# Kernel tuning notes

Hardware: AMD Instinct MI355X
Metric: run time of the kernel (lower is better)

## Reference

```python
import jax, jax.numpy as jnp
import numpy as np

N, R, E, EDIM = 500_000, 200, 1_000_000, 128


def setup_inputs() -> dict:
    key = jax.random.key(0)
    k = jax.random.split(key, 7)
    return {
        "emb": jax.random.normal(k[0], (N, EDIM), dtype=jnp.float32),
        "relations": jax.random.normal(k[1], (R, EDIM), dtype=jnp.float32),
        "tokeys": jax.random.normal(k[2], (EDIM, EDIM), dtype=jnp.float32) / np.sqrt(EDIM).astype(np.float32),
        "toqueries": jax.random.normal(k[3], (EDIM, EDIM), dtype=jnp.float32) / np.sqrt(EDIM).astype(np.float32),
        "si": jax.random.randint(k[4], (E,), 0, N),
        "pi": jax.random.randint(k[5], (E,), 0, R),
        "oi": jax.random.randint(k[6], (E,), 0, N),
    }


def reference(emb, relations, tokeys, toqueries, si, pi, oi):
    # emb: (N, e); relations: (R, e); tokeys/toqueries: (e, e); si/pi/oi: (E,)
    e = emb.shape[1]
    # einsum('ij, nj -> ni', W, x)  ==  x @ W.T
    semb = jnp.einsum('ij,nj->ni', tokeys, emb[si])      # (E, e)
    oemb = jnp.einsum('ij,nj->ni', toqueries, emb[oi])   # (E, e)
    pemb = relations[pi]                                  # (E, e)
    dots = jnp.sum(semb * pemb * oemb, axis=1) / jnp.sqrt(jnp.asarray(e, semb.dtype))
    return dots
```

## Files before the change

kernel.cpp:

```cpp
#include <hip/hip_runtime.h>
#include <hip/hip_bf16.h>

typedef __bf16 bf16x8 __attribute__((ext_vector_type(8)));
typedef float  f32x4  __attribute__((ext_vector_type(4)));

#define EDGES_TOTAL 1000000
#define TILE_E 16
#define TILES (EDGES_TOTAL / TILE_E)
#define EMB_ELEMS 64000000ULL
#define EMB_CHUNKS (EMB_ELEMS / 8)
#define WS_NEEDED (EMB_ELEMS * 2ULL)
#define GRID_BLOCKS 1280

__device__ __forceinline__ bf16x8 load_cvt8(const float* __restrict__ p) {
    f32x4 a = *(const f32x4*)p;
    f32x4 b = *(const f32x4*)(p + 4);
    bf16x8 r;
    r[0] = (__bf16)a[0]; r[1] = (__bf16)a[1]; r[2] = (__bf16)a[2]; r[3] = (__bf16)a[3];
    r[4] = (__bf16)b[0]; r[5] = (__bf16)b[1]; r[6] = (__bf16)b[2]; r[7] = (__bf16)b[3];
    return r;
}

__device__ __forceinline__ void gload_lds16(const void* g, void* l) {
    __builtin_amdgcn_global_load_lds(
        (const __attribute__((address_space(1))) void*)g,
        (__attribute__((address_space(3))) void*)l, 16, 0, 0);
}

__global__ __launch_bounds__(256) void cvt_bf16(
    const float* __restrict__ emb, __bf16* __restrict__ dst)
{
    const size_t stride = (size_t)gridDim.x * blockDim.x;
    for (size_t i = (size_t)blockIdx.x * blockDim.x + threadIdx.x; i < EMB_CHUNKS; i += stride) {
        size_t e = i * 8;
        *(bf16x8*)(dst + e) = load_cvt8(emb + e);
    }
}

__global__ __launch_bounds__(256, 5) void sampleall_staged(
    const __bf16* __restrict__ embb, const float* __restrict__ rel,
    const float* __restrict__ tokeys, const float* __restrict__ toqueries,
    const int* __restrict__ si, const int* __restrict__ pi, const int* __restrict__ oi,
    float* __restrict__ out)
{
    __shared__ __align__(16) __bf16 stage[2][32 * 128];
    __shared__ float red[4][16];

    const int tid  = threadIdx.x;
    const int lane = tid & 63;
    const int wid  = tid >> 6;
    const int c    = lane & 15;
    const int g    = lane >> 4;
    const int sub  = tid >> 4;
    const int gr   = tid & 15;

    bf16x8 wk[2][4], wq[2][4];
    #pragma unroll
    for (int tl = 0; tl < 2; ++tl) {
        const int row = (wid * 2 + tl) * 16 + c;
        #pragma unroll
        for (int j0 = 0; j0 < 4; ++j0) {
            wk[tl][j0] = load_cvt8(tokeys    + row * 128 + j0 * 32 + g * 8);
            wq[tl][j0] = load_cvt8(toqueries + row * 128 + j0 * 32 + g * 8);
        }
    }

    auto stage_issue = [&](int e0, int buf) {
        #pragma unroll
        for (int k = 0; k < 2; ++k) {
            const int r   = k * 16 + sub;
            const int idx = k ? oi[e0 + sub] : si[e0 + sub];
            const __bf16* src = embb + (size_t)idx * 128 + (gr ^ (r & 7)) * 8;
            __bf16* dst = &stage[buf][(k * 16 + (sub & ~3)) * 128];
            gload_lds16(src, dst);
        }
    };

    auto rdfrag = [&](int buf, int p, int j0) -> bf16x8 {
        const char* base = (const char*)&stage[buf][0];
        const int off = p * 256 + ((j0 * 64 + g * 16) ^ ((p & 7) << 4));
        return *(const bf16x8*)(base + off);
    };

    int tile = (int)blockIdx.x;
    stage_issue(tile * TILE_E, 0);
    __syncthreads();

    int b = 0;
    for (; tile < TILES; tile += GRID_BLOCKS) {
        const int nt = tile + GRID_BLOCKS;
        if (nt < TILES) stage_issue(nt * TILE_E, b ^ 1);

        const int e0 = tile * TILE_E;
        f32x4 aK[2], aQ[2];
        #pragma unroll
        for (int tl = 0; tl < 2; ++tl) {
            aK[tl] = (f32x4){0.f, 0.f, 0.f, 0.f};
            aQ[tl] = (f32x4){0.f, 0.f, 0.f, 0.f};
        }

        #pragma unroll
        for (int j0 = 0; j0 < 4; ++j0) {
            bf16x8 bs = rdfrag(b, c,      j0);
            bf16x8 bo = rdfrag(b, 16 + c, j0);
            #pragma unroll
            for (int tl = 0; tl < 2; ++tl) {
                aK[tl] = __builtin_amdgcn_mfma_f32_16x16x32_bf16(wk[tl][j0], bs, aK[tl], 0, 0, 0);
                aQ[tl] = __builtin_amdgcn_mfma_f32_16x16x32_bf16(wq[tl][j0], bo, aQ[tl], 0, 0, 0);
            }
        }

        const int pA = pi[e0 + c];
        float d0 = 0.f;
        #pragma unroll
        for (int tl = 0; tl < 2; ++tl) {
            const float* ra = rel + (size_t)pA * 128 + (wid * 2 + tl) * 16 + g * 4;
            f32x4 rA = *(const f32x4*)ra;
            #pragma unroll
            for (int r = 0; r < 4; ++r)
                d0 += aK[tl][r] * aQ[tl][r] * rA[r];
        }
        d0 += __shfl_xor(d0, 16); d0 += __shfl_xor(d0, 32);
        if (lane < 16) red[wid][c] = d0;

        __syncthreads();
        if (tid < 16) {
            const float s = red[0][tid] + red[1][tid] + red[2][tid] + red[3][tid];
            out[e0 + tid] = s * 0.08838834764831845f;
        }
        __syncthreads();
        b ^= 1;
    }
}

__global__ __launch_bounds__(256, 2) void sampleall_fused_f32(
    const float* __restrict__ emb, const float* __restrict__ rel,
    const float* __restrict__ tokeys, const float* __restrict__ toqueries,
    const int* __restrict__ si, const int* __restrict__ pi, const int* __restrict__ oi,
    float* __restrict__ out)
{
    __shared__ __align__(16) __bf16 ldsW[2][128 * 128];
    const int tid = threadIdx.x;
    #pragma unroll
    for (int it = 0; it < 16; ++it) {
        int gidx = tid + it * 256;
        int m    = gidx >> 11;
        int rm   = gidx & 2047;
        int row  = rm >> 4;
        int ch   = rm & 15;
        const float* src = (m ? toqueries : tokeys) + row * 128 + ch * 8;
        bf16x8 bv = load_cvt8(src);
        int byteoff = row * 256 + ((ch * 16) ^ ((row & 7) << 4));
        *(bf16x8*)((char*)(&ldsW[m][0]) + byteoff) = bv;
    }
    __syncthreads();

    const int lane = tid & 63;
    const int wid  = tid >> 6;
    const int c    = lane & 15;
    const int g    = lane >> 4;
    const int xm   = (c & 7) << 4;
    const char* wkbase = (const char*)(&ldsW[0][0]) + c * 256;
    const char* wqbase = (const char*)(&ldsW[1][0]) + c * 256;

    const int wtotal = (int)gridDim.x * 4;
    for (int tile = (int)blockIdx.x * 4 + wid; tile < EDGES_TOTAL / 32; tile += wtotal) {
        const int e0 = tile * 32;
        const int sA = si[e0 + c], sB = si[e0 + 16 + c];
        const int oA = oi[e0 + c], oB = oi[e0 + 16 + c];
        const int pA = pi[e0 + c], pB = pi[e0 + 16 + c];
        const float* ps0 = emb + (size_t)sA * 128 + g * 8;
        const float* ps1 = emb + (size_t)sB * 128 + g * 8;
        const float* po0 = emb + (size_t)oA * 128 + g * 8;
        const float* po1 = emb + (size_t)oB * 128 + g * 8;

        f32x4 accK0[8], accK1[8], accQ0[8], accQ1[8];
        #pragma unroll
        for (int t = 0; t < 8; ++t) {
            accK0[t] = (f32x4){0.f, 0.f, 0.f, 0.f};
            accK1[t] = (f32x4){0.f, 0.f, 0.f, 0.f};
            accQ0[t] = (f32x4){0.f, 0.f, 0.f, 0.f};
            accQ1[t] = (f32x4){0.f, 0.f, 0.f, 0.f};
        }
        #pragma unroll
        for (int j0 = 0; j0 < 4; ++j0) {
            bf16x8 bs0 = load_cvt8(ps0 + j0 * 32);
            bf16x8 bs1 = load_cvt8(ps1 + j0 * 32);
            bf16x8 bo0 = load_cvt8(po0 + j0 * 32);
            bf16x8 bo1 = load_cvt8(po1 + j0 * 32);
            const int offj = ((j0 * 64 + g * 16) ^ xm);
            #pragma unroll
            for (int t = 0; t < 8; ++t) {
                bf16x8 aK = *(const bf16x8*)(wkbase + t * 4096 + offj);
                accK0[t] = __builtin_amdgcn_mfma_f32_16x16x32_bf16(aK, bs0, accK0[t], 0, 0, 0);
                accK1[t] = __builtin_amdgcn_mfma_f32_16x16x32_bf16(aK, bs1, accK1[t], 0, 0, 0);
                bf16x8 aQ = *(const bf16x8*)(wqbase + t * 4096 + offj);
                accQ0[t] = __builtin_amdgcn_mfma_f32_16x16x32_bf16(aQ, bo0, accQ0[t], 0, 0, 0);
                accQ1[t] = __builtin_amdgcn_mfma_f32_16x16x32_bf16(aQ, bo1, accQ1[t], 0, 0, 0);
            }
        }
        float d0 = 0.f, d1 = 0.f;
        const float* relA = rel + (size_t)pA * 128 + g * 4;
        const float* relB = rel + (size_t)pB * 128 + g * 4;
        #pragma unroll
        for (int t = 0; t < 8; ++t) {
            f32x4 rA = *(const f32x4*)(relA + t * 16);
            f32x4 rB = *(const f32x4*)(relB + t * 16);
            #pragma unroll
            for (int r = 0; r < 4; ++r) {
                d0 += accK0[t][r] * accQ0[t][r] * rA[r];
                d1 += accK1[t][r] * accQ1[t][r] * rB[r];
            }
        }
        d0 += __shfl_xor(d0, 16); d0 += __shfl_xor(d0, 32);
        d1 += __shfl_xor(d1, 16); d1 += __shfl_xor(d1, 32);
        if (lane < 32) {
            const float inv_s = 0.08838834764831845f;
            out[e0 + lane] = (lane < 16 ? d0 : d1) * inv_s;
        }
    }
}

extern "C" void kernel_launch(void* const* d_in, const int* in_sizes, int n_in,
                              void* d_out, int out_size, void* d_ws, size_t ws_size,
                              hipStream_t stream)
{
    const float* emb = (const float*)d_in[0];
    const float* rel = (const float*)d_in[1];
    const float* tk  = (const float*)d_in[2];
    const float* tq  = (const float*)d_in[3];
    const int*   si  = (const int*)d_in[4];
    const int*   pi  = (const int*)d_in[5];
    const int*   oi  = (const int*)d_in[6];
    float* out = (float*)d_out;

    if (ws_size >= WS_NEEDED) {
        __bf16* embb = (__bf16*)d_ws;
        cvt_bf16<<<dim3(2048), dim3(256), 0, stream>>>(emb, embb);
        sampleall_staged<<<dim3(GRID_BLOCKS), dim3(256), 0, stream>>>(
            embb, rel, tk, tq, si, pi, oi, out);
    } else {
        sampleall_fused_f32<<<dim3(512), dim3(256), 0, stream>>>(emb, rel, tk, tq, si, pi, oi, out);
    }
}
```

Measured before the change: 248.7 us.

## Bucket-sort edges by subject index before bf16 gather-MFMA kernel

Adds a counting sort of edges by subject node (histogram, scan, scatter over 1024 buckets of 512 nodes), producing a permutation array. The main kernel then processes edges in bucket order, with each block taking a contiguous chunk of tiles, so subject-embedding gathers hit nearby rows and get better L2 locality. Results are written back through the permutation. This adds four small kernel launches and indirect loads of eidx, and the object gathers stay random, so it only helps if the subject-side locality outweighs the sort cost.

```diff
diff --git a/kernel.cpp b/kernel.cpp
--- a/kernel.cpp
+++ b/kernel.cpp
@@ -9,8 +9,19 @@
 #define TILES (EDGES_TOTAL / TILE_E)
 #define EMB_ELEMS 64000000ULL
 #define EMB_CHUNKS (EMB_ELEMS / 8)
-#define WS_NEEDED (EMB_ELEMS * 2ULL)
 #define GRID_BLOCKS 1280
+#define CHUNK ((TILES + GRID_BLOCKS - 1) / GRID_BLOCKS)
+
+#define NB 1024
+#define BSHIFT 9
+#define SORT_BLOCKS ((EDGES_TOTAL + 1023) / 1024)
+
+#define OFF_EMBB   0ULL
+#define OFF_COUNTS (EMB_ELEMS * 2ULL)
+#define OFF_CURSOR (OFF_COUNTS + NB * 4ULL)
+#define OFF_EIDX   (OFF_CURSOR + NB * 4ULL)
+#define WS_NEED_B  (OFF_EIDX + EDGES_TOTAL * 4ULL)
+#define WS_NEED_A  (EMB_ELEMS * 2ULL)
 
 __device__ __forceinline__ bf16x8 load_cvt8(const float* __restrict__ p) {
     f32x4 a = *(const f32x4*)p;
@@ -37,11 +48,90 @@
     }
 }
 
-__global__ __launch_bounds__(256, 5) void sampleall_staged(
+__global__ __launch_bounds__(256) void zero_counts(unsigned* __restrict__ counts) {
+    for (int i = threadIdx.x; i < NB; i += 256) counts[i] = 0;
+}
+
+__global__ __launch_bounds__(256) void hist_kernel(
+    const int* __restrict__ si, unsigned* __restrict__ counts)
+{
+    __shared__ unsigned lc[NB];
+    const int tid = threadIdx.x;
+    for (int i = tid; i < NB; i += 256) lc[i] = 0;
+    __syncthreads();
+    const int base = blockIdx.x * 1024;
+    #pragma unroll
+    for (int k = 0; k < 4; ++k) {
+        int e = base + k * 256 + tid;
+        if (e < EDGES_TOTAL) atomicAdd(&lc[((unsigned)si[e]) >> BSHIFT], 1u);
+    }
+    __syncthreads();
+    for (int i = tid; i < NB; i += 256)
+        if (lc[i]) atomicAdd(&counts[i], lc[i]);
+}
+
+__global__ __launch_bounds__(256) void scan_kernel(
+    unsigned* __restrict__ counts, unsigned* __restrict__ cursor)
+{
+    __shared__ unsigned ps[256];
+    const int t = threadIdx.x;
+    unsigned v[4], sum = 0;
+    #pragma unroll
+    for (int k = 0; k < 4; ++k) { v[k] = counts[t * 4 + k]; sum += v[k]; }
+    ps[t] = sum;
+    __syncthreads();
+    for (int off = 1; off < 256; off <<= 1) {
+        unsigned x = (t >= off) ? ps[t - off] : 0u;
+        __syncthreads();
+        ps[t] += x;
+        __syncthreads();
+    }
+    unsigned ex = t ? ps[t - 1] : 0u;
+    #pragma unroll
+    for (int k = 0; k < 4; ++k) {
+        unsigned c = v[k];
+        counts[t * 4 + k] = ex;
+        cursor[t * 4 + k] = ex;
+        ex += c;
+    }
+}
+
+__global__ __launch_bounds__(256) void scatter_kernel(
+    const int* __restrict__ si, unsigned* __restrict__ cursor, unsigned* __restrict__ eidx)
+{
+    __shared__ unsigned lc[NB];
+    const int tid = threadIdx.x;
+    for (int i = tid; i < NB; i += 256) lc[i] = 0;
+    __syncthreads();
+    const int base = blockIdx.x * 1024;
+    int b[4];
+    #pragma unroll
+    for (int k = 0; k < 4; ++k) {
+        int e = base + k * 256 + tid;
+        b[k] = -1;
+        if (e < EDGES_TOTAL) { b[k] = (int)(((unsigned)si[e]) >> BSHIFT); atomicAdd(&lc[b[k]], 1u); }
+    }
+    __syncthreads();
+    for (int i = tid; i < NB; i += 256) {
+        unsigned c = lc[i];
+        if (c) lc[i] = atomicAdd(&cursor[i], c);
+    }
+    __syncthreads();
+    #pragma unroll
+    for (int k = 0; k < 4; ++k) {
+        int e = base + k * 256 + tid;
+        if (e < EDGES_TOTAL) {
+            unsigned pos = atomicAdd(&lc[b[k]], 1u);
+            eidx[pos] = (unsigned)e;
+        }
+    }
+}
+
+__global__ __launch_bounds__(256, 5) void sampleall_bucketed(
     const __bf16* __restrict__ embb, const float* __restrict__ rel,
     const float* __restrict__ tokeys, const float* __restrict__ toqueries,
     const int* __restrict__ si, const int* __restrict__ pi, const int* __restrict__ oi,
-    float* __restrict__ out)
+    const unsigned* __restrict__ eidx, float* __restrict__ out)
 {
     __shared__ __align__(16) __bf16 stage[2][32 * 128];
     __shared__ float red[4][16];
@@ -66,6 +156,105 @@
     }
 
     auto stage_issue = [&](int e0, int buf) {
+        const int ed = (int)eidx[e0 + sub];
+        #pragma unroll
+        for (int k = 0; k < 2; ++k) {
+            const int r   = k * 16 + sub;
+            const int idx = k ? oi[ed] : si[ed];
+            const __bf16* src = embb + (size_t)idx * 128 + (gr ^ (r & 7)) * 8;
+            __bf16* dst = &stage[buf][(k * 16 + (sub & ~3)) * 128];
+            gload_lds16(src, dst);
+        }
+    };
+
+    auto rdfrag = [&](int buf, int p, int j0) -> bf16x8 {
+        const char* base = (const char*)&stage[buf][0];
+        const int off = p * 256 + ((j0 * 64 + g * 16) ^ ((p & 7) << 4));
+        return *(const bf16x8*)(base + off);
+    };
+
+    const int t0 = (int)blockIdx.x * CHUNK;
+    const int t1 = (t0 + CHUNK < TILES) ? t0 + CHUNK : TILES;
+    if (t0 >= t1) return;
+
+    stage_issue(t0 * TILE_E, 0);
+    __syncthreads();
+
+    int b = 0;
+    for (int tile = t0; tile < t1; ++tile) {
+        if (tile + 1 < t1) stage_issue((tile + 1) * TILE_E, b ^ 1);
+
+        const int e0 = tile * TILE_E;
+        f32x4 aK[2], aQ[2];
+        #pragma unroll
+        for (int tl = 0; tl < 2; ++tl) {
+            aK[tl] = (f32x4){0.f, 0.f, 0.f, 0.f};
+            aQ[tl] = (f32x4){0.f, 0.f, 0.f, 0.f};
+        }
+
+        #pragma unroll
+        for (int j0 = 0; j0 < 4; ++j0) {
+            bf16x8 bs = rdfrag(b, c,      j0);
+            bf16x8 bo = rdfrag(b, 16 + c, j0);
+            #pragma unroll
+            for (int tl = 0; tl < 2; ++tl) {
+                aK[tl] = __builtin_amdgcn_mfma_f32_16x16x32_bf16(wk[tl][j0], bs, aK[tl], 0, 0, 0);
+                aQ[tl] = __builtin_amdgcn_mfma_f32_16x16x32_bf16(wq[tl][j0], bo, aQ[tl], 0, 0, 0);
+            }
+        }
+
+        const int edc = (int)eidx[e0 + c];
+        const int pA  = pi[edc];
+        float d0 = 0.f;
+        #pragma unroll
+        for (int tl = 0; tl < 2; ++tl) {
+            f32x4 rA = *(const f32x4*)(rel + (size_t)pA * 128 + (wid * 2 + tl) * 16 + g * 4);
+            #pragma unroll
+            for (int r = 0; r < 4; ++r)
+                d0 += aK[tl][r] * aQ[tl][r] * rA[r];
+        }
+        d0 += __shfl_xor(d0, 16); d0 += __shfl_xor(d0, 32);
+        if (lane < 16) red[wid][c] = d0;
+
+        __syncthreads();
+        if (tid < 16) {
+            const float s = red[0][tid] + red[1][tid] + red[2][tid] + red[3][tid];
+            out[eidx[e0 + tid]] = s * 0.08838834764831845f;
+        }
+        __syncthreads();
+        b ^= 1;
+    }
+}
+
+__global__ __launch_bounds__(256, 5) void sampleall_staged(
+    const __bf16* __restrict__ embb, const float* __restrict__ rel,
+    const float* __restrict__ tokeys, const float* __restrict__ toqueries,
+    const int* __restrict__ si, const int* __restrict__ pi, const int* __restrict__ oi,
+    float* __restrict__ out)
+{
+    __shared__ __align__(16) __bf16 stage[2][32 * 128];
+    __shared__ float red[4][16];
+
+    const int tid  = threadIdx.x;
+    const int lane = tid & 63;
+    const int wid  = tid >> 6;
+    const int c    = lane & 15;
+    const int g    = lane >> 4;
+    const int sub  = tid >> 4;
+    const int gr   = tid & 15;
+
+    bf16x8 wk[2][4], wq[2][4];
+    #pragma unroll
+    for (int tl = 0; tl < 2; ++tl) {
+        const int row = (wid * 2 + tl) * 16 + c;
+        #pragma unroll
+        for (int j0 = 0; j0 < 4; ++j0) {
+            wk[tl][j0] = load_cvt8(tokeys    + row * 128 + j0 * 32 + g * 8);
+            wq[tl][j0] = load_cvt8(toqueries + row * 128 + j0 * 32 + g * 8);
+        }
+    }
+
+    auto stage_issue = [&](int e0, int buf) {
         #pragma unroll
         for (int k = 0; k < 2; ++k) {
             const int r   = k * 16 + sub;
@@ -98,7 +287,6 @@
             aK[tl] = (f32x4){0.f, 0.f, 0.f, 0.f};
             aQ[tl] = (f32x4){0.f, 0.f, 0.f, 0.f};
         }
-
         #pragma unroll
         for (int j0 = 0; j0 < 4; ++j0) {
             bf16x8 bs = rdfrag(b, c,      j0);
@@ -109,13 +297,11 @@
                 aQ[tl] = __builtin_amdgcn_mfma_f32_16x16x32_bf16(wq[tl][j0], bo, aQ[tl], 0, 0, 0);
             }
         }
-
         const int pA = pi[e0 + c];
         float d0 = 0.f;
         #pragma unroll
         for (int tl = 0; tl < 2; ++tl) {
-            const float* ra = rel + (size_t)pA * 128 + (wid * 2 + tl) * 16 + g * 4;
-            f32x4 rA = *(const f32x4*)ra;
+            f32x4 rA = *(const f32x4*)(rel + (size_t)pA * 128 + (wid * 2 + tl) * 16 + g * 4);
             #pragma unroll
             for (int r = 0; r < 4; ++r)
                 d0 += aK[tl][r] * aQ[tl][r] * rA[r];
@@ -234,7 +420,21 @@
     const int*   oi  = (const int*)d_in[6];
     float* out = (float*)d_out;
 
-    if (ws_size >= WS_NEEDED) {
+    if (ws_size >= WS_NEED_B) {
+        char* ws = (char*)d_ws;
+        __bf16*   embb   = (__bf16*)(ws + OFF_EMBB);
+        unsigned* counts = (unsigned*)(ws + OFF_COUNTS);
+        unsigned* cursor = (unsigned*)(ws + OFF_CURSOR);
+        unsigned* eidx   = (unsigned*)(ws + OFF_EIDX);
+
+        cvt_bf16<<<dim3(2048), dim3(256), 0, stream>>>(emb, embb);
+        zero_counts<<<dim3(1), dim3(256), 0, stream>>>(counts);
+        hist_kernel<<<dim3(SORT_BLOCKS), dim3(256), 0, stream>>>(si, counts);
+        scan_kernel<<<dim3(1), dim3(256), 0, stream>>>(counts, cursor);
+        scatter_kernel<<<dim3(SORT_BLOCKS), dim3(256), 0, stream>>>(si, cursor, eidx);
+        sampleall_bucketed<<<dim3(GRID_BLOCKS), dim3(256), 0, stream>>>(
+            embb, rel, tk, tq, si, pi, oi, eidx, out);
+    } else if (ws_size >= WS_NEED_A) {
         __bf16* embb = (__bf16*)d_ws;
         cvt_bf16<<<dim3(2048), dim3(256), 0, stream>>>(emb, embb);
         sampleall_staged<<<dim3(GRID_BLOCKS), dim3(256), 0, stream>>>(
```

After: 421.2 us. +69.4%, slower.
